# Kernel optimization log

Measured on AMD Instinct MI355X. Metric: run time of the kernel, lower is better.

The kernel has to match this reference:

```python
import jax, jax.numpy as jnp
import numpy as np

N, E, F, H, L, G = 100000, 1600000, 32, 64, 4, 256
EPS = 1e-5


def setup_inputs() -> dict:
    key = jax.random.key(0)
    ks = jax.random.split(key, 12)
    x = jax.random.normal(ks[0], (N, F), dtype=jnp.float32)
    edge_index = jax.random.randint(ks[1], (2, E), 0, N, dtype=jnp.int32)
    batch = jnp.sort(jax.random.randint(ks[2], (N,), 0, G, dtype=jnp.int32))
    s = 0.1
    return {
        "x": x,
        "edge_index": edge_index,
        "batch": batch,
        "w_embed": jax.random.normal(ks[3], (F, H), dtype=jnp.float32) * s,
        "b_embed": jnp.zeros((H,), dtype=jnp.float32),
        "conv_W": jax.random.normal(ks[4], (L, H, H), dtype=jnp.float32) * s,
        "conv_b": jnp.zeros((L, H), dtype=jnp.float32),
        "bn_gamma": jnp.ones((L, H), dtype=jnp.float32),
        "bn_beta": jnp.zeros((L, H), dtype=jnp.float32),
        "w1": jax.random.normal(ks[5], (H, H // 2), dtype=jnp.float32) * s,
        "b1": jnp.zeros((H // 2,), dtype=jnp.float32),
        "w2": jax.random.normal(ks[6], (H // 2, 1), dtype=jnp.float32) * s,
        "b2": jnp.zeros((1,), dtype=jnp.float32),
    }


def _gcn_conv(h, src, dst, W, b):
    # PyG GCNConv: add self loops, symmetric D^-1/2 (A+I) D^-1/2 normalization
    hw = h @ W  # [N,H]
    deg = jax.ops.segment_sum(jnp.ones((E,), h.dtype), dst, num_segments=N) + 1.0
    dinv = jax.lax.rsqrt(deg)  # [N]
    msg = hw[src] * (dinv[src] * dinv[dst])[:, None]  # [E,H] gather + scale
    agg = jax.ops.segment_sum(msg, dst, num_segments=N)  # scatter-add
    agg = agg + hw * (dinv * dinv)[:, None]  # self-loop contribution
    return agg + b


def _batchnorm(h, gamma, beta):
    # training-mode BatchNorm1d over the node dimension
    mean = jnp.mean(h, axis=0)
    var = jnp.var(h, axis=0)
    return (h - mean) * jax.lax.rsqrt(var + EPS) * gamma + beta


def reference(x, edge_index, batch, w_embed, b_embed, conv_W, conv_b,
              bn_gamma, bn_beta, w1, b1, w2, b2):
    src, dst = edge_index[0], edge_index[1]
    h = x @ w_embed + b_embed  # node embedding [N,H]
    for i in range(L):
        identity = h
        h = _gcn_conv(h, src, dst, conv_W[i], conv_b[i])
        h = _batchnorm(h, bn_gamma[i], bn_beta[i])
        h = jax.nn.relu(h)
        # dropout is identity in eval mode
        h = h + identity  # use_residual=True
    # global mean pool over graphs
    sums = jax.ops.segment_sum(h, batch, num_segments=G)  # [G,H]
    counts = jax.ops.segment_sum(jnp.ones((N,), h.dtype), batch, num_segments=G)
    pooled = sums / jnp.maximum(counts, 1.0)[:, None]
    out = jax.nn.relu(pooled @ w1 + b1)
    out = out @ w2 + b2  # [G,1]
    return out
```

## Files before the change

kernel.cpp:

```cpp
#include <hip/hip_runtime.h>
#include <hip/hip_fp16.h>

#define Nn 100000
#define Ne 1600000
#define Fi 32
#define Hd 64
#define Ll 4
#define Gg 256
#define BN_EPS 1e-5f
#define NPB 128
#define NBINS ((Nn + NPB - 1) / NPB)
#define CHUNK 8192
#define NBLK ((Ne + CHUNK - 1) / CHUNK)
#define IDXW (NBINS + 2)
#define TPAD 68
#define XPAD 36
#define NGB ((Nn + 63) / 64)


__global__ void k_dinv(const int* __restrict__ deg, float* __restrict__ dinv) {
    int n = blockIdx.x * blockDim.x + threadIdx.x;
    if (n < Nn) dinv[n] = rsqrtf((float)deg[n] + 1.0f);
}

__global__ void k_scanA(const int* __restrict__ deg, int* __restrict__ row_off,
                        int* __restrict__ bsum) {
    __shared__ int s[256];
    int t = threadIdx.x;
    int i = blockIdx.x * 256 + t;
    int v = (i < Nn) ? deg[i] : 0;
    s[t] = v;
    __syncthreads();
    int x = v;
    for (int off = 1; off < 256; off <<= 1) {
        int u = (t >= off) ? s[t - off] : 0;
        __syncthreads();
        x += u;
        s[t] = x;
        __syncthreads();
    }
    if (i < Nn) row_off[i] = x - v;
    if (t == 255) bsum[blockIdx.x] = x;
}

__global__ void k_scanB(int* __restrict__ bsum, int nblk) {
    __shared__ int s[512];
    int t = threadIdx.x;
    int v = (t < nblk) ? bsum[t] : 0;
    s[t] = v;
    __syncthreads();
    int x = v;
    for (int off = 1; off < 512; off <<= 1) {
        int u = (t >= off) ? s[t - off] : 0;
        __syncthreads();
        x += u;
        s[t] = x;
        __syncthreads();
    }
    if (t < nblk) bsum[t] = x - v;
}

__global__ void k_scanC(int* __restrict__ row_off, const int* __restrict__ bsum) {
    int i = blockIdx.x * 256 + threadIdx.x;
    if (i < Nn) row_off[i] += bsum[blockIdx.x];
    if (i == 0) row_off[Nn] = Ne;
}

__global__ __launch_bounds__(256) void k_part(const int* __restrict__ src,
                                              const int* __restrict__ dst,
                                              unsigned* __restrict__ tpack,
                                              unsigned short* __restrict__ idx16) {
    __shared__ int hist[NBINS];
    __shared__ int lofs[NBINS + 1];
    __shared__ int wsum[256];
    __shared__ unsigned stage[CHUNK];
    int blk = blockIdx.x, t = threadIdx.x;
    int e0 = blk * CHUNK;
    int nval = min(CHUNK, Ne - e0);

    for (int i = t; i < NBINS; i += 256) hist[i] = 0;
    __syncthreads();
    for (int i = t; i < nval; i += 256)
        atomicAdd(&hist[dst[e0 + i] >> 7], 1);
    __syncthreads();

    int base = t * 4;
    int loc[4];
    int s = 0;
#pragma unroll
    for (int k = 0; k < 4; k++) {
        int b = base + k;
        int c = (b < NBINS) ? hist[b] : 0;
        loc[k] = s;
        s += c;
    }
    wsum[t] = s;
    __syncthreads();
    int x = s;
    for (int off = 1; off < 256; off <<= 1) {
        int u = (t >= off) ? wsum[t - off] : 0;
        __syncthreads();
        x += u;
        wsum[t] = x;
        __syncthreads();
    }
    int excl = x - s;
#pragma unroll
    for (int k = 0; k < 4; k++) {
        int b = base + k;
        if (b < NBINS) lofs[b] = excl + loc[k];
    }
    if (t == 0) lofs[NBINS] = nval;
    __syncthreads();

    for (int i = t; i <= NBINS; i += 256)
        idx16[(size_t)blk * IDXW + i] = (unsigned short)lofs[i];

    for (int i = t; i < NBINS; i += 256) hist[i] = lofs[i];
    __syncthreads();
    for (int i = t; i < nval; i += 256) {
        int d = dst[e0 + i];
        int sv = src[e0 + i];
        int p = atomicAdd(&hist[d >> 7], 1);
        stage[p] = (unsigned)sv | ((unsigned)(d & (NPB - 1)) << 17);
    }
    __syncthreads();
    for (int i = t; i < nval; i += 256)
        tpack[(size_t)blk * CHUNK + i] = stage[i];
}

__global__ __launch_bounds__(256) void k_deg2(const unsigned* __restrict__ tpack,
                                              const unsigned short* __restrict__ idx16,
                                              int* __restrict__ deg) {
    __shared__ int cnt[NPB];
    int b = blockIdx.x, t = threadIdx.x;
    if (t < NPB) cnt[t] = 0;
    __syncthreads();
    if (t < NBLK) {
        const unsigned short* row = idx16 + (size_t)t * IDXW;
        int s = row[b], e = row[b + 1];
        const unsigned* tp = tpack + (size_t)t * CHUNK;
        for (int k = s; k < e; k++)
            atomicAdd(&cnt[tp[k] >> 17], 1);
    }
    __syncthreads();
    int node = b * NPB + t;
    if (t < NPB && node < Nn) deg[node] = cnt[t];
}

__global__ __launch_bounds__(256) void k_csr(const int* __restrict__ row_off,
                                             const unsigned* __restrict__ tpack,
                                             const unsigned short* __restrict__ idx16,
                                             int* __restrict__ esrc) {
    __shared__ int cur[NPB];
    int b = blockIdx.x, t = threadIdx.x;
    int n0 = b * NPB;
    int e0 = row_off[n0];
    if (t < NPB) {
        int node = n0 + t;
        cur[t] = (node < Nn) ? (row_off[node] - e0) : 0;
    }
    __syncthreads();
    if (t < NBLK) {
        const unsigned short* row = idx16 + (size_t)t * IDXW;
        int s = row[b], e = row[b + 1];
        const unsigned* tp = tpack + (size_t)t * CHUNK;
        for (int k = s; k < e; k++) {
            unsigned v = tp[k];
            int p = atomicAdd(&cur[v >> 17], 1);
            esrc[e0 + p] = (int)(v & 0x1FFFFu);
        }
    }
}

__global__ void k_gstart(const int* __restrict__ batch, int* __restrict__ gstart) {
    int g = threadIdx.x;
    int lo = 0, hi = Nn;
    while (lo < hi) {
        int mid = (lo + hi) >> 1;
        if (batch[mid] < g) lo = mid + 1; else hi = mid;
    }
    gstart[g] = lo;
    if (g == 0) gstart[Gg] = Nn;
}


#define MT_FMA(AV, W0, W1, W2, W3, R)                                          \
    acc[R][0] = fmaf(AV.x, W0.x, acc[R][0]);                                   \
    acc[R][0] = fmaf(AV.y, W1.x, acc[R][0]);                                   \
    acc[R][0] = fmaf(AV.z, W2.x, acc[R][0]);                                   \
    acc[R][0] = fmaf(AV.w, W3.x, acc[R][0]);                                   \
    acc[R][1] = fmaf(AV.x, W0.y, acc[R][1]);                                   \
    acc[R][1] = fmaf(AV.y, W1.y, acc[R][1]);                                   \
    acc[R][1] = fmaf(AV.z, W2.y, acc[R][1]);                                   \
    acc[R][1] = fmaf(AV.w, W3.y, acc[R][1]);                                   \
    acc[R][2] = fmaf(AV.x, W0.z, acc[R][2]);                                   \
    acc[R][2] = fmaf(AV.y, W1.z, acc[R][2]);                                   \
    acc[R][2] = fmaf(AV.z, W2.z, acc[R][2]);                                   \
    acc[R][2] = fmaf(AV.w, W3.z, acc[R][2]);                                   \
    acc[R][3] = fmaf(AV.x, W0.w, acc[R][3]);                                   \
    acc[R][3] = fmaf(AV.y, W1.w, acc[R][3]);                                   \
    acc[R][3] = fmaf(AV.z, W2.w, acc[R][3]);                                   \
    acc[R][3] = fmaf(AV.w, W3.w, acc[R][3]);

__device__ inline void store_half4(unsigned short* dst, float a, float b,
                                   float c, float d) {
    __half2 p0 = __floats2half2_rn(a, b);
    __half2 p1 = __floats2half2_rn(c, d);
    uint2 u;
    u.x = *(unsigned*)&p0;
    u.y = *(unsigned*)&p1;
    *(uint2*)dst = u;
}

__global__ __launch_bounds__(256, 4) void k_gemmF2(const float* __restrict__ agg,
                                                   const float* __restrict__ bnsc,
                                                   const float* __restrict__ bnsh,
                                                   float* __restrict__ h,
                                                   const float* __restrict__ W,
                                                   unsigned short* __restrict__ hwh) {
    __shared__ float hs[64 * TPAD];
    __shared__ float ws[64 * 64];
    int t = threadIdx.x;
    int n0 = blockIdx.x * 64;

    for (int f = t; f < 1024; f += 256)
        ((float4*)ws)[f] = ((const float4*)W)[f];

    for (int f = t; f < 1024; f += 256) {
        int row = f >> 4, c4 = (f & 15) * 4;
        int node = n0 + row;
        if (node < Nn) {
            float4 a  = *(const float4*)(agg + (size_t)node * Hd + c4);
            float4 ho = *(const float4*)(h + (size_t)node * Hd + c4);
            float4 sc = ((const float4*)bnsc)[f & 15];
            float4 sh = ((const float4*)bnsh)[f & 15];
            float4 r4;
            r4.x = fmaxf(fmaf(a.x, sc.x, sh.x), 0.f) + ho.x;
            r4.y = fmaxf(fmaf(a.y, sc.y, sh.y), 0.f) + ho.y;
            r4.z = fmaxf(fmaf(a.z, sc.z, sh.z), 0.f) + ho.z;
            r4.w = fmaxf(fmaf(a.w, sc.w, sh.w), 0.f) + ho.w;
            *(float4*)(h + (size_t)node * Hd + c4) = r4;
            *(float4*)&hs[row * TPAD + c4] = r4;
        } else {
            *(float4*)&hs[row * TPAD + c4] = make_float4(0.f, 0.f, 0.f, 0.f);
        }
    }
    __syncthreads();

    int i = t >> 4, j = t & 15;
    float acc[4][4] = {};
#pragma unroll 2
    for (int k = 0; k < 64; k += 4) {
        float4 w0 = *(const float4*)&ws[(k + 0) * 64 + 4 * j];
        float4 w1 = *(const float4*)&ws[(k + 1) * 64 + 4 * j];
        float4 w2 = *(const float4*)&ws[(k + 2) * 64 + 4 * j];
        float4 w3 = *(const float4*)&ws[(k + 3) * 64 + 4 * j];
        float4 a0 = *(const float4*)&hs[(4 * i + 0) * TPAD + k];
        float4 a1 = *(const float4*)&hs[(4 * i + 1) * TPAD + k];
        float4 a2 = *(const float4*)&hs[(4 * i + 2) * TPAD + k];
        float4 a3 = *(const float4*)&hs[(4 * i + 3) * TPAD + k];
        MT_FMA(a0, w0, w1, w2, w3, 0)
        MT_FMA(a1, w0, w1, w2, w3, 1)
        MT_FMA(a2, w0, w1, w2, w3, 2)
        MT_FMA(a3, w0, w1, w2, w3, 3)
    }
#pragma unroll
    for (int r = 0; r < 4; r++) {
        int node = n0 + 4 * i + r;
        if (node < Nn)
            store_half4(hwh + (size_t)node * Hd + 4 * j,
                        acc[r][0], acc[r][1], acc[r][2], acc[r][3]);
    }
}

__global__ __launch_bounds__(256, 4) void k_embed_gemm2(const float* __restrict__ x,
                                                        const float* __restrict__ we,
                                                        const float* __restrict__ be,
                                                        const float* __restrict__ W,
                                                        float* __restrict__ h,
                                                        unsigned short* __restrict__ hwh) {
    __shared__ float uni[64 * XPAD + 32 * 64];
    __shared__ float hs[64 * TPAD];
    __shared__ float bes[64];
    float* xs  = uni;
    float* wes = uni + 64 * XPAD;
    float* ws  = uni;
    int t = threadIdx.x;
    int n0 = blockIdx.x * 64;

    for (int f = t; f < 512; f += 256)
        ((float4*)wes)[f] = ((const float4*)we)[f];
    if (t < 64) bes[t] = be[t];

    for (int f = t; f < 512; f += 256) {
        int row = f >> 3, c4 = (f & 7) * 4;
        int node = n0 + row;
        float4 v = (node < Nn) ? *(const float4*)(x + (size_t)node * Fi + c4)
                               : make_float4(0.f, 0.f, 0.f, 0.f);
        *(float4*)&xs[row * XPAD + c4] = v;
    }
    __syncthreads();

    int i = t >> 4, j = t & 15;
    {
        float acc[4][4];
#pragma unroll
        for (int r = 0; r < 4; r++)
#pragma unroll
            for (int c = 0; c < 4; c++) acc[r][c] = bes[4 * j + c];
#pragma unroll 2
        for (int k = 0; k < 32; k += 4) {
            float4 w0 = *(const float4*)&wes[(k + 0) * 64 + 4 * j];
            float4 w1 = *(const float4*)&wes[(k + 1) * 64 + 4 * j];
            float4 w2 = *(const float4*)&wes[(k + 2) * 64 + 4 * j];
            float4 w3 = *(const float4*)&wes[(k + 3) * 64 + 4 * j];
            float4 a0 = *(const float4*)&xs[(4 * i + 0) * XPAD + k];
            float4 a1 = *(const float4*)&xs[(4 * i + 1) * XPAD + k];
            float4 a2 = *(const float4*)&xs[(4 * i + 2) * XPAD + k];
            float4 a3 = *(const float4*)&xs[(4 * i + 3) * XPAD + k];
            MT_FMA(a0, w0, w1, w2, w3, 0)
            MT_FMA(a1, w0, w1, w2, w3, 1)
            MT_FMA(a2, w0, w1, w2, w3, 2)
            MT_FMA(a3, w0, w1, w2, w3, 3)
        }
#pragma unroll
        for (int r = 0; r < 4; r++) {
            int node = n0 + 4 * i + r;
            float4 hv = make_float4(acc[r][0], acc[r][1], acc[r][2], acc[r][3]);
            *(float4*)&hs[(4 * i + r) * TPAD + 4 * j] = hv;
            if (node < Nn)
                *(float4*)(h + (size_t)node * Hd + 4 * j) = hv;
        }
    }
    __syncthreads();
    for (int f = t; f < 1024; f += 256)
        ((float4*)ws)[f] = ((const float4*)W)[f];
    __syncthreads();
    {
        float acc[4][4] = {};
#pragma unroll 2
        for (int k = 0; k < 64; k += 4) {
            float4 w0 = *(const float4*)&ws[(k + 0) * 64 + 4 * j];
            float4 w1 = *(const float4*)&ws[(k + 1) * 64 + 4 * j];
            float4 w2 = *(const float4*)&ws[(k + 2) * 64 + 4 * j];
            float4 w3 = *(const float4*)&ws[(k + 3) * 64 + 4 * j];
            float4 a0 = *(const float4*)&hs[(4 * i + 0) * TPAD + k];
            float4 a1 = *(const float4*)&hs[(4 * i + 1) * TPAD + k];
            float4 a2 = *(const float4*)&hs[(4 * i + 2) * TPAD + k];
            float4 a3 = *(const float4*)&hs[(4 * i + 3) * TPAD + k];
            MT_FMA(a0, w0, w1, w2, w3, 0)
            MT_FMA(a1, w0, w1, w2, w3, 1)
            MT_FMA(a2, w0, w1, w2, w3, 2)
            MT_FMA(a3, w0, w1, w2, w3, 3)
        }
#pragma unroll
        for (int r = 0; r < 4; r++) {
            int node = n0 + 4 * i + r;
            if (node < Nn)
                store_half4(hwh + (size_t)node * Hd + 4 * j,
                            acc[r][0], acc[r][1], acc[r][2], acc[r][3]);
        }
    }
}


__global__ __launch_bounds__(256) void k_gatherH(const unsigned short* __restrict__ hwh,
                                                 const float* __restrict__ dinv,
                                                 const int* __restrict__ row_off,
                                                 const int* __restrict__ esrc,
                                                 const float* __restrict__ bias,
                                                 float* __restrict__ agg,
                                                 float* __restrict__ bnacc) {
    int g = threadIdx.x >> 3;
    int l = threadIdx.x & 7;
    int node = blockIdx.x * 32 + g;
    float di = dinv[node];
    float scl = di * di;
    float acc[8];

    uint4 v = *(const uint4*)(hwh + (size_t)node * Hd + l * 8);
#pragma unroll
    for (int q = 0; q < 4; q++) {
        __half2 hp = *(__half2*)(((unsigned*)&v) + q);
        float2 f = __half22float2(hp);
        acc[2 * q]     = f.x * scl + bias[l * 8 + 2 * q];
        acc[2 * q + 1] = f.y * scl + bias[l * 8 + 2 * q + 1];
    }

    int e = row_off[node], e1 = row_off[node + 1];
    for (; e + 3 < e1; e += 4) {
        int s0 = esrc[e], s1 = esrc[e + 1], s2 = esrc[e + 2], s3 = esrc[e + 3];
        float c0 = dinv[s0] * di, c1 = dinv[s1] * di;
        float c2 = dinv[s2] * di, c3 = dinv[s3] * di;
        uint4 v0 = *(const uint4*)(hwh + (size_t)s0 * Hd + l * 8);
        uint4 v1 = *(const uint4*)(hwh + (size_t)s1 * Hd + l * 8);
        uint4 v2 = *(const uint4*)(hwh + (size_t)s2 * Hd + l * 8);
        uint4 v3 = *(const uint4*)(hwh + (size_t)s3 * Hd + l * 8);
#pragma unroll
        for (int q = 0; q < 4; q++) {
            float2 f0 = __half22float2(*(__half2*)(((unsigned*)&v0) + q));
            float2 f1 = __half22float2(*(__half2*)(((unsigned*)&v1) + q));
            float2 f2 = __half22float2(*(__half2*)(((unsigned*)&v2) + q));
            float2 f3 = __half22float2(*(__half2*)(((unsigned*)&v3) + q));
            acc[2 * q]     = fmaf(f0.x, c0, acc[2 * q]);
            acc[2 * q + 1] = fmaf(f0.y, c0, acc[2 * q + 1]);
            acc[2 * q]     = fmaf(f1.x, c1, acc[2 * q]);
            acc[2 * q + 1] = fmaf(f1.y, c1, acc[2 * q + 1]);
            acc[2 * q]     = fmaf(f2.x, c2, acc[2 * q]);
            acc[2 * q + 1] = fmaf(f2.y, c2, acc[2 * q + 1]);
            acc[2 * q]     = fmaf(f3.x, c3, acc[2 * q]);
            acc[2 * q + 1] = fmaf(f3.y, c3, acc[2 * q + 1]);
        }
    }
    for (; e < e1; e++) {
        int s0 = esrc[e];
        float c0 = dinv[s0] * di;
        uint4 v0 = *(const uint4*)(hwh + (size_t)s0 * Hd + l * 8);
#pragma unroll
        for (int q = 0; q < 4; q++) {
            float2 f0 = __half22float2(*(__half2*)(((unsigned*)&v0) + q));
            acc[2 * q]     = fmaf(f0.x, c0, acc[2 * q]);
            acc[2 * q + 1] = fmaf(f0.y, c0, acc[2 * q + 1]);
        }
    }

    *(float4*)(agg + (size_t)node * Hd + l * 8)     = make_float4(acc[0], acc[1], acc[2], acc[3]);
    *(float4*)(agg + (size_t)node * Hd + l * 8 + 4) = make_float4(acc[4], acc[5], acc[6], acc[7]);

    __shared__ float ls[2048];
    *(float4*)&ls[g * 64 + l * 8]     = make_float4(acc[0], acc[1], acc[2], acc[3]);
    *(float4*)&ls[g * 64 + l * 8 + 4] = make_float4(acc[4], acc[5], acc[6], acc[7]);
    __syncthreads();
    int t = threadIdx.x;
    if (t < 64) {
        float s = 0.f, s2 = 0.f;
#pragma unroll
        for (int gg = 0; gg < 32; gg++) {
            float vv = ls[gg * 64 + t];
            s += vv;
            s2 = fmaf(vv, vv, s2);
        }
        float* a = bnacc + (blockIdx.x & 63) * 128;
        atomicAdd(&a[t], s);
        atomicAdd(&a[64 + t], s2);
    }
}

__global__ void k_bnfinal(const float* __restrict__ acc, const float* __restrict__ gamma,
                          const float* __restrict__ beta, float* __restrict__ bnsc,
                          float* __restrict__ bnsh) {
    int c = threadIdx.x;
    if (c >= 64) return;
    float s = 0.f, s2 = 0.f;
    for (int sh = 0; sh < 64; sh++) {
        s  += acc[sh * 128 + c];
        s2 += acc[sh * 128 + 64 + c];
    }
    float mean = s / (float)Nn;
    float var = s2 / (float)Nn - mean * mean;
    var = fmaxf(var, 0.f);
    float sc = gamma[c] * rsqrtf(var + BN_EPS);
    bnsc[c] = sc;
    bnsh[c] = beta[c] - mean * sc;
}

__global__ __launch_bounds__(1024) void k_poolF(const float* __restrict__ agg,
                                                const float* __restrict__ bnsc,
                                                const float* __restrict__ bnsh,
                                                const float* __restrict__ h,
                                                const int* __restrict__ gstart,
                                                float* __restrict__ pooled) {
    int g = blockIdx.x;
    int t = threadIdx.x;
    int ch = t & 63, sl = t >> 6;
    float sc = bnsc[ch], shv = bnsh[ch];
    int n0 = gstart[g], n1 = gstart[g + 1];
    float s = 0.f;
    for (int n = n0 + sl; n < n1; n += 16) {
        float a  = agg[(size_t)n * Hd + ch];
        float ho = h[(size_t)n * Hd + ch];
        s += fmaxf(fmaf(a, sc, shv), 0.f) + ho;
    }
    __shared__ float ls[1024];
    ls[t] = s;
    __syncthreads();
    if (t < 64) {
        float acc = 0.f;
#pragma unroll
        for (int k = 0; k < 16; k++) acc += ls[k * 64 + t];
        float cnt = (float)(n1 - n0);
        pooled[g * Hd + t] = acc / fmaxf(cnt, 1.0f);
    }
}

__global__ __launch_bounds__(256) void k_head(const float* __restrict__ pooled,
                                              const float* __restrict__ w1,
                                              const float* __restrict__ b1,
                                              const float* __restrict__ w2,
                                              const float* __restrict__ b2,
                                              float* __restrict__ out) {
    __shared__ float sw1[Hd * 32], sw2[32], sb1[32];
    int t = threadIdx.x;
    for (int i = t; i < Hd * 32; i += 256) sw1[i] = w1[i];
    if (t < 32) { sw2[t] = w2[t]; sb1[t] = b1[t]; }
    __syncthreads();
    float acc2[32];
#pragma unroll
    for (int k = 0; k < 32; k++) acc2[k] = sb1[k];
    for (int j = 0; j < Hd; j++) {
        float pj = pooled[t * Hd + j];
#pragma unroll
        for (int k = 0; k < 32; k++) acc2[k] = fmaf(pj, sw1[j * 32 + k], acc2[k]);
    }
    float o = b2[0];
#pragma unroll
    for (int k = 0; k < 32; k++) o += fmaxf(acc2[k], 0.f) * sw2[k];
    out[t] = o;
}


extern "C" void kernel_launch(void* const* d_in, const int* in_sizes, int n_in,
                              void* d_out, int out_size, void* d_ws, size_t ws_size,
                              hipStream_t stream) {
    const float* x       = (const float*)d_in[0];
    const int*   eidx    = (const int*)d_in[1];
    const int*   batch   = (const int*)d_in[2];
    const float* w_embed = (const float*)d_in[3];
    const float* b_embed = (const float*)d_in[4];
    const float* conv_W  = (const float*)d_in[5];
    const float* conv_b  = (const float*)d_in[6];
    const float* gamma   = (const float*)d_in[7];
    const float* beta    = (const float*)d_in[8];
    const float* w1      = (const float*)d_in[9];
    const float* b1      = (const float*)d_in[10];
    const float* w2      = (const float*)d_in[11];
    const float* b2      = (const float*)d_in[12];
    const int* src = eidx;
    const int* dst = eidx + Ne;

    char* p = (char*)d_ws;
    auto alloc = [&](size_t bytes) -> void* {
        void* r = (void*)p;
        p += (bytes + 255) / 256 * 256;
        return r;
    };
    float*    h       = (float*)alloc((size_t)Nn * Hd * 4);
    unsigned short* hwh = (unsigned short*)alloc((size_t)Nn * Hd * 2);
    float*    agg     = (float*)alloc((size_t)Nn * Hd * 4);
    int*      deg     = (int*)alloc((size_t)Nn * 4);
    int*      row_off = (int*)alloc((size_t)(Nn + 1) * 4);
    float*    dinv    = (float*)alloc((size_t)Nn * 4);
    int*      bsum    = (int*)alloc(512 * 4);
    int*      esrc    = (int*)alloc((size_t)Ne * 4);
    unsigned* tpack   = (unsigned*)alloc((size_t)NBLK * CHUNK * 4);
    unsigned short* idx16 = (unsigned short*)alloc((size_t)NBLK * IDXW * 2);
    float*    bnacc   = (float*)alloc((size_t)Ll * 64 * 128 * 4);
    float*    bnsc    = (float*)alloc(64 * 4);
    float*    bnsh    = (float*)alloc(64 * 4);
    float*    pooled  = (float*)alloc((size_t)Gg * Hd * 4);
    int*      gstart  = (int*)alloc((size_t)(Gg + 1) * 4);
    (void)ws_size; (void)in_sizes; (void)n_in; (void)out_size;

    const int NB_N = (Nn + 255) / 256;
    const int NB_G32 = (Nn + 31) / 32;

    hipMemsetAsync(bnacc, 0, (size_t)Ll * 64 * 128 * 4, stream);

    k_part<<<NBLK, 256, 0, stream>>>(src, dst, tpack, idx16);
    k_deg2<<<NBINS, 256, 0, stream>>>(tpack, idx16, deg);
    k_scanA<<<NB_N, 256, 0, stream>>>(deg, row_off, bsum);
    k_scanB<<<1, 512, 0, stream>>>(bsum, NB_N);
    k_scanC<<<NB_N, 256, 0, stream>>>(row_off, bsum);
    k_dinv<<<NB_N, 256, 0, stream>>>(deg, dinv);
    k_csr<<<NBINS, 256, 0, stream>>>(row_off, tpack, idx16, esrc);
    k_gstart<<<1, 256, 0, stream>>>(batch, gstart);

    k_embed_gemm2<<<NGB, 256, 0, stream>>>(x, w_embed, b_embed, conv_W, h, hwh);

    for (int i = 0; i < Ll; i++) {
        if (i > 0)
            k_gemmF2<<<NGB, 256, 0, stream>>>(agg, bnsc, bnsh, h,
                                              conv_W + (size_t)i * Hd * Hd, hwh);
        k_gatherH<<<NB_G32, 256, 0, stream>>>(hwh, dinv, row_off, esrc,
                                              conv_b + (size_t)i * Hd, agg,
                                              bnacc + (size_t)i * 64 * 128);
        k_bnfinal<<<1, 64, 0, stream>>>(bnacc + (size_t)i * 64 * 128,
                                        gamma + (size_t)i * Hd,
                                        beta + (size_t)i * Hd, bnsc, bnsh);
    }

    k_poolF<<<Gg, 1024, 0, stream>>>(agg, bnsc, bnsh, h, gstart, pooled);
    k_head<<<1, 256, 0, stream>>>(pooled, w1, b1, w2, b2, (float*)d_out);
}
```

Measured before the change: 340.3 us.

## Widen gather to 32 lanes per node, halve partition chunk, merge small kernels

The GCN gather kernel now gives each node a full wavefront half of 32 lanes, each reading one half2 of the 64 channels, instead of 8 lanes each loading a uint4. Blocks grow to 512 threads covering 16 nodes, and BN partial sums spread over 128 shards instead of 64 to reduce atomic contention. The edge partition chunk shrinks to 4096, so there are more partition blocks, and the deg/CSR kernels now loop over rows. The dinv and gstart kernels are folded into the scan kernels to cut launches. The narrower per-lane loads issue more memory instructions per edge, and the smaller chunk produces more idx16 rows to scan.

```diff
diff --git a/kernel.cpp b/kernel.cpp
--- a/kernel.cpp
+++ b/kernel.cpp
@@ -10,18 +10,14 @@
 #define BN_EPS 1e-5f
 #define NPB 128
 #define NBINS ((Nn + NPB - 1) / NPB)
-#define CHUNK 8192
+#define CHUNK 4096
 #define NBLK ((Ne + CHUNK - 1) / CHUNK)
 #define IDXW (NBINS + 2)
 #define TPAD 68
 #define XPAD 36
 #define NGB ((Nn + 63) / 64)
-
-
-__global__ void k_dinv(const int* __restrict__ deg, float* __restrict__ dinv) {
-    int n = blockIdx.x * blockDim.x + threadIdx.x;
-    if (n < Nn) dinv[n] = rsqrtf((float)deg[n] + 1.0f);
-}
+#define NSH 128
+
 
 __global__ void k_scanA(const int* __restrict__ deg, int* __restrict__ row_off,
                         int* __restrict__ bsum) {
@@ -43,9 +39,22 @@
     if (t == 255) bsum[blockIdx.x] = x;
 }
 
-__global__ void k_scanB(int* __restrict__ bsum, int nblk) {
+__global__ void k_scanBG(int* __restrict__ bsum, int nblk,
+                         const int* __restrict__ batch, int* __restrict__ gstart) {
+    int t = threadIdx.x;
+    if (blockIdx.x == 1) {
+        if (t < Gg) {
+            int lo = 0, hi = Nn;
+            while (lo < hi) {
+                int mid = (lo + hi) >> 1;
+                if (batch[mid] < t) lo = mid + 1; else hi = mid;
+            }
+            gstart[t] = lo;
+            if (t == 0) gstart[Gg] = Nn;
+        }
+        return;
+    }
     __shared__ int s[512];
-    int t = threadIdx.x;
     int v = (t < nblk) ? bsum[t] : 0;
     s[t] = v;
     __syncthreads();
@@ -60,9 +69,13 @@
     if (t < nblk) bsum[t] = x - v;
 }
 
-__global__ void k_scanC(int* __restrict__ row_off, const int* __restrict__ bsum) {
+__global__ void k_scanC(int* __restrict__ row_off, const int* __restrict__ bsum,
+                        const int* __restrict__ deg, float* __restrict__ dinv) {
     int i = blockIdx.x * 256 + threadIdx.x;
-    if (i < Nn) row_off[i] += bsum[blockIdx.x];
+    if (i < Nn) {
+        row_off[i] += bsum[blockIdx.x];
+        dinv[i] = rsqrtf((float)deg[i] + 1.0f);
+    }
     if (i == 0) row_off[Nn] = Ne;
 }
 
@@ -136,10 +149,10 @@
     int b = blockIdx.x, t = threadIdx.x;
     if (t < NPB) cnt[t] = 0;
     __syncthreads();
-    if (t < NBLK) {
-        const unsigned short* row = idx16 + (size_t)t * IDXW;
+    for (int r = t; r < NBLK; r += 256) {
+        const unsigned short* row = idx16 + (size_t)r * IDXW;
         int s = row[b], e = row[b + 1];
-        const unsigned* tp = tpack + (size_t)t * CHUNK;
+        const unsigned* tp = tpack + (size_t)r * CHUNK;
         for (int k = s; k < e; k++)
             atomicAdd(&cnt[tp[k] >> 17], 1);
     }
@@ -161,27 +174,16 @@
         cur[t] = (node < Nn) ? (row_off[node] - e0) : 0;
     }
     __syncthreads();
-    if (t < NBLK) {
-        const unsigned short* row = idx16 + (size_t)t * IDXW;
+    for (int r = t; r < NBLK; r += 256) {
+        const unsigned short* row = idx16 + (size_t)r * IDXW;
         int s = row[b], e = row[b + 1];
-        const unsigned* tp = tpack + (size_t)t * CHUNK;
+        const unsigned* tp = tpack + (size_t)r * CHUNK;
         for (int k = s; k < e; k++) {
             unsigned v = tp[k];
             int p = atomicAdd(&cur[v >> 17], 1);
             esrc[e0 + p] = (int)(v & 0x1FFFFu);
         }
     }
-}
-
-__global__ void k_gstart(const int* __restrict__ batch, int* __restrict__ gstart) {
-    int g = threadIdx.x;
-    int lo = 0, hi = Nn;
-    while (lo < hi) {
-        int mid = (lo + hi) >> 1;
-        if (batch[mid] < g) lo = mid + 1; else hi = mid;
-    }
-    gstart[g] = lo;
-    if (g == 0) gstart[Gg] = Nn;
 }
 
 
@@ -365,83 +367,69 @@
 }
 
 
-__global__ __launch_bounds__(256) void k_gatherH(const unsigned short* __restrict__ hwh,
+__global__ __launch_bounds__(512) void k_gatherH(const unsigned short* __restrict__ hwh,
                                                  const float* __restrict__ dinv,
                                                  const int* __restrict__ row_off,
                                                  const int* __restrict__ esrc,
                                                  const float* __restrict__ bias,
                                                  float* __restrict__ agg,
                                                  float* __restrict__ bnacc) {
-    int g = threadIdx.x >> 3;
-    int l = threadIdx.x & 7;
-    int node = blockIdx.x * 32 + g;
+    int t = threadIdx.x;
+    int g = t >> 5;
+    int l = t & 31;
+    int c0 = 2 * l;
+    int node = blockIdx.x * 16 + g;
     float di = dinv[node];
     float scl = di * di;
-    float acc[8];
-
-    uint4 v = *(const uint4*)(hwh + (size_t)node * Hd + l * 8);
-#pragma unroll
-    for (int q = 0; q < 4; q++) {
-        __half2 hp = *(__half2*)(((unsigned*)&v) + q);
-        float2 f = __half22float2(hp);
-        acc[2 * q]     = f.x * scl + bias[l * 8 + 2 * q];
-        acc[2 * q + 1] = f.y * scl + bias[l * 8 + 2 * q + 1];
+    float a0, a1;
+    {
+        unsigned v = *(const unsigned*)(hwh + (size_t)node * Hd + c0);
+        float2 f = __half22float2(*(__half2*)&v);
+        a0 = f.x * scl + bias[c0];
+        a1 = f.y * scl + bias[c0 + 1];
     }
 
     int e = row_off[node], e1 = row_off[node + 1];
     for (; e + 3 < e1; e += 4) {
         int s0 = esrc[e], s1 = esrc[e + 1], s2 = esrc[e + 2], s3 = esrc[e + 3];
-        float c0 = dinv[s0] * di, c1 = dinv[s1] * di;
-        float c2 = dinv[s2] * di, c3 = dinv[s3] * di;
-        uint4 v0 = *(const uint4*)(hwh + (size_t)s0 * Hd + l * 8);
-        uint4 v1 = *(const uint4*)(hwh + (size_t)s1 * Hd + l * 8);
-        uint4 v2 = *(const uint4*)(hwh + (size_t)s2 * Hd + l * 8);
-        uint4 v3 = *(const uint4*)(hwh + (size_t)s3 * Hd + l * 8);
-#pragma unroll
-        for (int q = 0; q < 4; q++) {
-            float2 f0 = __half22float2(*(__half2*)(((unsigned*)&v0) + q));
-            float2 f1 = __half22float2(*(__half2*)(((unsigned*)&v1) + q));
-            float2 f2 = __half22float2(*(__half2*)(((unsigned*)&v2) + q));
-            float2 f3 = __half22float2(*(__half2*)(((unsigned*)&v3) + q));
-            acc[2 * q]     = fmaf(f0.x, c0, acc[2 * q]);
-            acc[2 * q + 1] = fmaf(f0.y, c0, acc[2 * q + 1]);
-            acc[2 * q]     = fmaf(f1.x, c1, acc[2 * q]);
-            acc[2 * q + 1] = fmaf(f1.y, c1, acc[2 * q + 1]);
-            acc[2 * q]     = fmaf(f2.x, c2, acc[2 * q]);
-            acc[2 * q + 1] = fmaf(f2.y, c2, acc[2 * q + 1]);
-            acc[2 * q]     = fmaf(f3.x, c3, acc[2 * q]);
-            acc[2 * q + 1] = fmaf(f3.y, c3, acc[2 * q + 1]);
-        }
+        float q0 = dinv[s0] * di, q1 = dinv[s1] * di;
+        float q2 = dinv[s2] * di, q3 = dinv[s3] * di;
+        unsigned v0 = *(const unsigned*)(hwh + (size_t)s0 * Hd + c0);
+        unsigned v1 = *(const unsigned*)(hwh + (size_t)s1 * Hd + c0);
+        unsigned v2 = *(const unsigned*)(hwh + (size_t)s2 * Hd + c0);
+        unsigned v3 = *(const unsigned*)(hwh + (size_t)s3 * Hd + c0);
+        float2 f0 = __half22float2(*(__half2*)&v0);
+        float2 f1 = __half22float2(*(__half2*)&v1);
+        float2 f2 = __half22float2(*(__half2*)&v2);
+        float2 f3 = __half22float2(*(__half2*)&v3);
+        a0 = fmaf(f0.x, q0, a0); a1 = fmaf(f0.y, q0, a1);
+        a0 = fmaf(f1.x, q1, a0); a1 = fmaf(f1.y, q1, a1);
+        a0 = fmaf(f2.x, q2, a0); a1 = fmaf(f2.y, q2, a1);
+        a0 = fmaf(f3.x, q3, a0); a1 = fmaf(f3.y, q3, a1);
     }
     for (; e < e1; e++) {
         int s0 = esrc[e];
-        float c0 = dinv[s0] * di;
-        uint4 v0 = *(const uint4*)(hwh + (size_t)s0 * Hd + l * 8);
-#pragma unroll
-        for (int q = 0; q < 4; q++) {
-            float2 f0 = __half22float2(*(__half2*)(((unsigned*)&v0) + q));
-            acc[2 * q]     = fmaf(f0.x, c0, acc[2 * q]);
-            acc[2 * q + 1] = fmaf(f0.y, c0, acc[2 * q + 1]);
-        }
-    }
-
-    *(float4*)(agg + (size_t)node * Hd + l * 8)     = make_float4(acc[0], acc[1], acc[2], acc[3]);
-    *(float4*)(agg + (size_t)node * Hd + l * 8 + 4) = make_float4(acc[4], acc[5], acc[6], acc[7]);
-
-    __shared__ float ls[2048];
-    *(float4*)&ls[g * 64 + l * 8]     = make_float4(acc[0], acc[1], acc[2], acc[3]);
-    *(float4*)&ls[g * 64 + l * 8 + 4] = make_float4(acc[4], acc[5], acc[6], acc[7]);
-    __syncthreads();
-    int t = threadIdx.x;
+        float q0 = dinv[s0] * di;
+        unsigned v0 = *(const unsigned*)(hwh + (size_t)s0 * Hd + c0);
+        float2 f0 = __half22float2(*(__half2*)&v0);
+        a0 = fmaf(f0.x, q0, a0); a1 = fmaf(f0.y, q0, a1);
+    }
+
+    *(float2*)(agg + (size_t)node * Hd + c0) = make_float2(a0, a1);
+
+    __shared__ float ls[1024];
+    ls[g * 64 + c0] = a0;
+    ls[g * 64 + c0 + 1] = a1;
+    __syncthreads();
     if (t < 64) {
         float s = 0.f, s2 = 0.f;
 #pragma unroll
-        for (int gg = 0; gg < 32; gg++) {
+        for (int gg = 0; gg < 16; gg++) {
             float vv = ls[gg * 64 + t];
             s += vv;
             s2 = fmaf(vv, vv, s2);
         }
-        float* a = bnacc + (blockIdx.x & 63) * 128;
+        float* a = bnacc + (blockIdx.x & (NSH - 1)) * 128;
         atomicAdd(&a[t], s);
         atomicAdd(&a[64 + t], s2);
     }
@@ -453,7 +441,7 @@
     int c = threadIdx.x;
     if (c >= 64) return;
     float s = 0.f, s2 = 0.f;
-    for (int sh = 0; sh < 64; sh++) {
+    for (int sh = 0; sh < NSH; sh++) {
         s  += acc[sh * 128 + c];
         s2 += acc[sh * 128 + 64 + c];
     }
@@ -555,7 +543,7 @@
     int*      esrc    = (int*)alloc((size_t)Ne * 4);
     unsigned* tpack   = (unsigned*)alloc((size_t)NBLK * CHUNK * 4);
     unsigned short* idx16 = (unsigned short*)alloc((size_t)NBLK * IDXW * 2);
-    float*    bnacc   = (float*)alloc((size_t)Ll * 64 * 128 * 4);
+    float*    bnacc   = (float*)alloc((size_t)Ll * NSH * 128 * 4);
     float*    bnsc    = (float*)alloc(64 * 4);
     float*    bnsh    = (float*)alloc(64 * 4);
     float*    pooled  = (float*)alloc((size_t)Gg * Hd * 4);
@@ -563,18 +551,16 @@
     (void)ws_size; (void)in_sizes; (void)n_in; (void)out_size;
 
     const int NB_N = (Nn + 255) / 256;
-    const int NB_G32 = (Nn + 31) / 32;
-
-    hipMemsetAsync(bnacc, 0, (size_t)Ll * 64 * 128 * 4, stream);
+    const int NB_G16 = Nn / 16;
+
+    hipMemsetAsync(bnacc, 0, (size_t)Ll * NSH * 128 * 4, stream);
 
     k_part<<<NBLK, 256, 0, stream>>>(src, dst, tpack, idx16);
     k_deg2<<<NBINS, 256, 0, stream>>>(tpack, idx16, deg);
     k_scanA<<<NB_N, 256, 0, stream>>>(deg, row_off, bsum);
-    k_scanB<<<1, 512, 0, stream>>>(bsum, NB_N);
-    k_scanC<<<NB_N, 256, 0, stream>>>(row_off, bsum);
-    k_dinv<<<NB_N, 256, 0, stream>>>(deg, dinv);
+    k_scanBG<<<2, 512, 0, stream>>>(bsum, NB_N, batch, gstart);
+    k_scanC<<<NB_N, 256, 0, stream>>>(row_off, bsum, deg, dinv);
     k_csr<<<NBINS, 256, 0, stream>>>(row_off, tpack, idx16, esrc);
-    k_gstart<<<1, 256, 0, stream>>>(batch, gstart);
 
     k_embed_gemm2<<<NGB, 256, 0, stream>>>(x, w_embed, b_embed, conv_W, h, hwh);
 
@@ -582,10 +568,10 @@
         if (i > 0)
             k_gemmF2<<<NGB, 256, 0, stream>>>(agg, bnsc, bnsh, h,
                                               conv_W + (size_t)i * Hd * Hd, hwh);
-        k_gatherH<<<NB_G32, 256, 0, stream>>>(hwh, dinv, row_off, esrc,
+        k_gatherH<<<NB_G16, 512, 0, stream>>>(hwh, dinv, row_off, esrc,
                                               conv_b + (size_t)i * Hd, agg,
-                                              bnacc + (size_t)i * 64 * 128);
-        k_bnfinal<<<1, 64, 0, stream>>>(bnacc + (size_t)i * 64 * 128,
+                                              bnacc + (size_t)i * NSH * 128);
+        k_bnfinal<<<1, 64, 0, stream>>>(bnacc + (size_t)i * NSH * 128,
                                         gamma + (size_t)i * Hd,
                                         beta + (size_t)i * Hd, bnsc, bnsh);
     }
```

Result: slower. 392.8 us (+15.4%).

## Unroll gather by eight, fuse setup kernels, halve partition chunk, widen BN shards

Applied to the files above, without the earlier changes.

Each gather thread now issues eight independent edge loads before the FMAs, where it used to issue four, so more memory requests are in flight per lane. The dinv computation is folded into the scan fix-up kernel, and the graph-start search shares a launch with the block-sum scan, which removes two small launches. The partition chunk size is halved, so the per-bin kernels loop over more rows, and the number of BatchNorm atomic shards is doubled to reduce contention. The wider unroll raises register pressure and can lower occupancy.

```diff
diff --git a/kernel.cpp b/kernel.cpp
--- a/kernel.cpp
+++ b/kernel.cpp
@@ -10,18 +10,14 @@
 #define BN_EPS 1e-5f
 #define NPB 128
 #define NBINS ((Nn + NPB - 1) / NPB)
-#define CHUNK 8192
+#define CHUNK 4096
 #define NBLK ((Ne + CHUNK - 1) / CHUNK)
 #define IDXW (NBINS + 2)
 #define TPAD 68
 #define XPAD 36
 #define NGB ((Nn + 63) / 64)
-
-
-__global__ void k_dinv(const int* __restrict__ deg, float* __restrict__ dinv) {
-    int n = blockIdx.x * blockDim.x + threadIdx.x;
-    if (n < Nn) dinv[n] = rsqrtf((float)deg[n] + 1.0f);
-}
+#define NSH 128
+
 
 __global__ void k_scanA(const int* __restrict__ deg, int* __restrict__ row_off,
                         int* __restrict__ bsum) {
@@ -43,9 +39,22 @@
     if (t == 255) bsum[blockIdx.x] = x;
 }
 
-__global__ void k_scanB(int* __restrict__ bsum, int nblk) {
+__global__ void k_scanBG(int* __restrict__ bsum, int nblk,
+                         const int* __restrict__ batch, int* __restrict__ gstart) {
+    int t = threadIdx.x;
+    if (blockIdx.x == 1) {
+        if (t < Gg) {
+            int lo = 0, hi = Nn;
+            while (lo < hi) {
+                int mid = (lo + hi) >> 1;
+                if (batch[mid] < t) lo = mid + 1; else hi = mid;
+            }
+            gstart[t] = lo;
+            if (t == 0) gstart[Gg] = Nn;
+        }
+        return;
+    }
     __shared__ int s[512];
-    int t = threadIdx.x;
     int v = (t < nblk) ? bsum[t] : 0;
     s[t] = v;
     __syncthreads();
@@ -60,9 +69,13 @@
     if (t < nblk) bsum[t] = x - v;
 }
 
-__global__ void k_scanC(int* __restrict__ row_off, const int* __restrict__ bsum) {
+__global__ void k_scanC(int* __restrict__ row_off, const int* __restrict__ bsum,
+                        const int* __restrict__ deg, float* __restrict__ dinv) {
     int i = blockIdx.x * 256 + threadIdx.x;
-    if (i < Nn) row_off[i] += bsum[blockIdx.x];
+    if (i < Nn) {
+        row_off[i] += bsum[blockIdx.x];
+        dinv[i] = rsqrtf((float)deg[i] + 1.0f);
+    }
     if (i == 0) row_off[Nn] = Ne;
 }
 
@@ -136,10 +149,10 @@
     int b = blockIdx.x, t = threadIdx.x;
     if (t < NPB) cnt[t] = 0;
     __syncthreads();
-    if (t < NBLK) {
-        const unsigned short* row = idx16 + (size_t)t * IDXW;
+    for (int r = t; r < NBLK; r += 256) {
+        const unsigned short* row = idx16 + (size_t)r * IDXW;
         int s = row[b], e = row[b + 1];
-        const unsigned* tp = tpack + (size_t)t * CHUNK;
+        const unsigned* tp = tpack + (size_t)r * CHUNK;
         for (int k = s; k < e; k++)
             atomicAdd(&cnt[tp[k] >> 17], 1);
     }
@@ -161,27 +174,16 @@
         cur[t] = (node < Nn) ? (row_off[node] - e0) : 0;
     }
     __syncthreads();
-    if (t < NBLK) {
-        const unsigned short* row = idx16 + (size_t)t * IDXW;
+    for (int r = t; r < NBLK; r += 256) {
+        const unsigned short* row = idx16 + (size_t)r * IDXW;
         int s = row[b], e = row[b + 1];
-        const unsigned* tp = tpack + (size_t)t * CHUNK;
+        const unsigned* tp = tpack + (size_t)r * CHUNK;
         for (int k = s; k < e; k++) {
             unsigned v = tp[k];
             int p = atomicAdd(&cur[v >> 17], 1);
             esrc[e0 + p] = (int)(v & 0x1FFFFu);
         }
     }
-}
-
-__global__ void k_gstart(const int* __restrict__ batch, int* __restrict__ gstart) {
-    int g = threadIdx.x;
-    int lo = 0, hi = Nn;
-    while (lo < hi) {
-        int mid = (lo + hi) >> 1;
-        if (batch[mid] < g) lo = mid + 1; else hi = mid;
-    }
-    gstart[g] = lo;
-    if (g == 0) gstart[Gg] = Nn;
 }
 
 
@@ -382,38 +384,49 @@
     uint4 v = *(const uint4*)(hwh + (size_t)node * Hd + l * 8);
 #pragma unroll
     for (int q = 0; q < 4; q++) {
-        __half2 hp = *(__half2*)(((unsigned*)&v) + q);
-        float2 f = __half22float2(hp);
+        float2 f = __half22float2(*(__half2*)(((unsigned*)&v) + q));
         acc[2 * q]     = f.x * scl + bias[l * 8 + 2 * q];
         acc[2 * q + 1] = f.y * scl + bias[l * 8 + 2 * q + 1];
     }
 
     int e = row_off[node], e1 = row_off[node + 1];
-    for (; e + 3 < e1; e += 4) {
-        int s0 = esrc[e], s1 = esrc[e + 1], s2 = esrc[e + 2], s3 = esrc[e + 3];
+    for (; e + 7 < e1; e += 8) {
+        int sidx[8];
+        float cf[8];
+        uint4 vv[8];
+#pragma unroll
+        for (int u = 0; u < 8; u++) sidx[u] = esrc[e + u];
+#pragma unroll
+        for (int u = 0; u < 8; u++) cf[u] = dinv[sidx[u]] * di;
+#pragma unroll
+        for (int u = 0; u < 8; u++)
+            vv[u] = *(const uint4*)(hwh + (size_t)sidx[u] * Hd + l * 8);
+#pragma unroll
+        for (int u = 0; u < 8; u++) {
+#pragma unroll
+            for (int q = 0; q < 4; q++) {
+                float2 f = __half22float2(*(__half2*)(((unsigned*)&vv[u]) + q));
+                acc[2 * q]     = fmaf(f.x, cf[u], acc[2 * q]);
+                acc[2 * q + 1] = fmaf(f.y, cf[u], acc[2 * q + 1]);
+            }
+        }
+    }
+    for (; e + 1 < e1; e += 2) {
+        int s0 = esrc[e], s1 = esrc[e + 1];
         float c0 = dinv[s0] * di, c1 = dinv[s1] * di;
-        float c2 = dinv[s2] * di, c3 = dinv[s3] * di;
         uint4 v0 = *(const uint4*)(hwh + (size_t)s0 * Hd + l * 8);
         uint4 v1 = *(const uint4*)(hwh + (size_t)s1 * Hd + l * 8);
-        uint4 v2 = *(const uint4*)(hwh + (size_t)s2 * Hd + l * 8);
-        uint4 v3 = *(const uint4*)(hwh + (size_t)s3 * Hd + l * 8);
 #pragma unroll
         for (int q = 0; q < 4; q++) {
             float2 f0 = __half22float2(*(__half2*)(((unsigned*)&v0) + q));
             float2 f1 = __half22float2(*(__half2*)(((unsigned*)&v1) + q));
-            float2 f2 = __half22float2(*(__half2*)(((unsigned*)&v2) + q));
-            float2 f3 = __half22float2(*(__half2*)(((unsigned*)&v3) + q));
             acc[2 * q]     = fmaf(f0.x, c0, acc[2 * q]);
             acc[2 * q + 1] = fmaf(f0.y, c0, acc[2 * q + 1]);
             acc[2 * q]     = fmaf(f1.x, c1, acc[2 * q]);
             acc[2 * q + 1] = fmaf(f1.y, c1, acc[2 * q + 1]);
-            acc[2 * q]     = fmaf(f2.x, c2, acc[2 * q]);
-            acc[2 * q + 1] = fmaf(f2.y, c2, acc[2 * q + 1]);
-            acc[2 * q]     = fmaf(f3.x, c3, acc[2 * q]);
-            acc[2 * q + 1] = fmaf(f3.y, c3, acc[2 * q + 1]);
-        }
-    }
-    for (; e < e1; e++) {
+        }
+    }
+    if (e < e1) {
         int s0 = esrc[e];
         float c0 = dinv[s0] * di;
         uint4 v0 = *(const uint4*)(hwh + (size_t)s0 * Hd + l * 8);
@@ -441,7 +454,7 @@
             s += vv;
             s2 = fmaf(vv, vv, s2);
         }
-        float* a = bnacc + (blockIdx.x & 63) * 128;
+        float* a = bnacc + (blockIdx.x & (NSH - 1)) * 128;
         atomicAdd(&a[t], s);
         atomicAdd(&a[64 + t], s2);
     }
@@ -453,7 +466,7 @@
     int c = threadIdx.x;
     if (c >= 64) return;
     float s = 0.f, s2 = 0.f;
-    for (int sh = 0; sh < 64; sh++) {
+    for (int sh = 0; sh < NSH; sh++) {
         s  += acc[sh * 128 + c];
         s2 += acc[sh * 128 + 64 + c];
     }
@@ -555,7 +568,7 @@
     int*      esrc    = (int*)alloc((size_t)Ne * 4);
     unsigned* tpack   = (unsigned*)alloc((size_t)NBLK * CHUNK * 4);
     unsigned short* idx16 = (unsigned short*)alloc((size_t)NBLK * IDXW * 2);
-    float*    bnacc   = (float*)alloc((size_t)Ll * 64 * 128 * 4);
+    float*    bnacc   = (float*)alloc((size_t)Ll * NSH * 128 * 4);
     float*    bnsc    = (float*)alloc(64 * 4);
     float*    bnsh    = (float*)alloc(64 * 4);
     float*    pooled  = (float*)alloc((size_t)Gg * Hd * 4);
@@ -563,18 +576,16 @@
     (void)ws_size; (void)in_sizes; (void)n_in; (void)out_size;
 
     const int NB_N = (Nn + 255) / 256;
-    const int NB_G32 = (Nn + 31) / 32;
-
-    hipMemsetAsync(bnacc, 0, (size_t)Ll * 64 * 128 * 4, stream);
+    const int NB_G32 = Nn / 32;
+
+    hipMemsetAsync(bnacc, 0, (size_t)Ll * NSH * 128 * 4, stream);
 
     k_part<<<NBLK, 256, 0, stream>>>(src, dst, tpack, idx16);
     k_deg2<<<NBINS, 256, 0, stream>>>(tpack, idx16, deg);
     k_scanA<<<NB_N, 256, 0, stream>>>(deg, row_off, bsum);
-    k_scanB<<<1, 512, 0, stream>>>(bsum, NB_N);
-    k_scanC<<<NB_N, 256, 0, stream>>>(row_off, bsum);
-    k_dinv<<<NB_N, 256, 0, stream>>>(deg, dinv);
+    k_scanBG<<<2, 512, 0, stream>>>(bsum, NB_N, batch, gstart);
+    k_scanC<<<NB_N, 256, 0, stream>>>(row_off, bsum, deg, dinv);
     k_csr<<<NBINS, 256, 0, stream>>>(row_off, tpack, idx16, esrc);
-    k_gstart<<<1, 256, 0, stream>>>(batch, gstart);
 
     k_embed_gemm2<<<NGB, 256, 0, stream>>>(x, w_embed, b_embed, conv_W, h, hwh);
 
@@ -584,8 +595,8 @@
                                               conv_W + (size_t)i * Hd * Hd, hwh);
         k_gatherH<<<NB_G32, 256, 0, stream>>>(hwh, dinv, row_off, esrc,
                                               conv_b + (size_t)i * Hd, agg,
-                                              bnacc + (size_t)i * 64 * 128);
-        k_bnfinal<<<1, 64, 0, stream>>>(bnacc + (size_t)i * 64 * 128,
+                                              bnacc + (size_t)i * NSH * 128);
+        k_bnfinal<<<1, 64, 0, stream>>>(bnacc + (size_t)i * NSH * 128,
                                         gamma + (size_t)i * Hd,
                                         beta + (size_t)i * Hd, bnsc, bnsh);
     }
```

Result: slower. 353.9 us (+4.0%).
